# Optimization experiments

Hardware: AMD Instinct MI355X
Metric: run time of the kernel (lower is better)

The kernel has to match this reference:

```python
import jax, jax.numpy as jnp
import numpy as np

B, C, H, W = 16, 256, 64, 32
HID = C // 8  # down_ratio = 8
NEG = -9e15   # masking constant from the original code


def _spatial_adj(h, w):
    # 8-connected grid adjacency over n = h*w pixels (no self loops), as bool [n, n]
    ii, jj = np.meshgrid(np.arange(h), np.arange(w), indexing='ij')
    pi, pj = ii.reshape(-1), jj.reshape(-1)
    di = np.abs(pi[:, None] - pi[None, :])
    dj = np.abs(pj[:, None] - pj[None, :])
    return (di <= 1) & (dj <= 1) & ~((di == 0) & (dj == 0))


def _channel_adj(c):
    # chain adjacency over channels: |i - j| == 1, bool [c, c]
    i = np.arange(c)
    return np.abs(i[:, None] - i[None, :]) == 1


def setup_inputs() -> dict:
    key = jax.random.key(0)
    ks = jax.random.split(key, 12)
    return {
        'x': jax.random.normal(ks[0], (B, C, H, W), dtype=jnp.float32),
        'wa': jax.random.normal(ks[1], (HID, C), dtype=jnp.float32) * 0.05,
        'ga': jax.random.uniform(ks[2], (HID,), dtype=jnp.float32) + 0.5,
        'ba': jax.random.normal(ks[3], (HID,), dtype=jnp.float32) * 0.1,
        'ma': jnp.zeros((HID,), dtype=jnp.float32),
        'va': jnp.ones((HID,), dtype=jnp.float32),
        'ws': jax.random.normal(ks[4], (HID, C), dtype=jnp.float32) * 0.05,
        'gs': jax.random.uniform(ks[5], (HID,), dtype=jnp.float32) + 0.5,
        'bs': jax.random.normal(ks[6], (HID,), dtype=jnp.float32) * 0.1,
        'ms': jnp.zeros((HID,), dtype=jnp.float32),
        'vs': jnp.ones((HID,), dtype=jnp.float32),
        'gama': jax.random.uniform(ks[7], (1,), dtype=jnp.float32),
    }


def _bn_relu(y, g, b, m, v):
    # eval-mode BatchNorm2d (+ReLU) on [B, k, H, W]
    inv = g / jnp.sqrt(v + 1e-5)
    return jax.nn.relu(y * inv[:, None, None] + (b - m * inv)[:, None, None])


def reference(x, wa, ga, ba, ma, va, ws, gs, bs, ms, vs, gama):
    b, c, h, w = x.shape
    n = h * w
    adj = jnp.asarray(_spatial_adj(h, w))   # [n, n] bool (constant)
    cadj = jnp.asarray(_channel_adj(c))     # [c, c] bool (constant)

    # spatial GAT branch
    alpha = _bn_relu(jnp.einsum('bchw,oc->bohw', x, wa), ga, ba, ma, va)
    sigma = _bn_relu(jnp.einsum('bchw,oc->bohw', x, ws), gs, bs, ms, vs)
    xf = x.reshape(b, c, n)
    af = alpha.reshape(b, -1, n)            # [b, hid, n]
    sf = sigma.reshape(b, -1, n)            # [b, hid, n]
    att = jnp.einsum('bkn,bkm->bnm', af, sf)              # [b, n, n]
    att = jax.nn.softmax(jnp.where(adj, att, NEG), axis=2)
    h_s = jnp.einsum('bnm,bcm->bcn', att, xf).reshape(b, c, h, w)

    # channel GAT branch
    Gc = jnp.einsum('bcn,bdn->bcd', xf, xf)               # [b, c, c]
    catt = jax.nn.softmax(jnp.where(cadj, Gc, NEG), axis=2)
    h_p = jnp.einsum('bcd,bdn->bcn', catt, xf).reshape(b, c, h, w)

    h_prime = jax.nn.elu(h_s + h_p)
    return (1.0 - gama) * x + gama * h_prime
```

## Files before the change

### kernel.cpp

```cpp
#include <hip/hip_runtime.h>
#include <math.h>

#define BB 16
#define CC 256
#define HH 64
#define WW 32
#define NN (HH*WW)
#define NEGC (-9e15f)
#define CPAD 136

typedef __attribute__((ext_vector_type(8))) short bf16x8;
typedef __attribute__((ext_vector_type(4))) float f32x4;

__device__ float g_wlo[BB*CC];
__device__ float g_whi[BB*CC];
__device__ float g_as[(size_t)BB*NN*64];
__device__ float g_part[BB*32*256];
__device__ float g_w8[(size_t)BB*NN*8];

__device__ __forceinline__ unsigned short f2bf(float f) {
    unsigned int u = __float_as_uint(f);
    u += 0x7FFFu + ((u >> 16) & 1u);
    return (unsigned short)(u >> 16);
}

__global__ __launch_bounds__(256) void k_gemm(
        const float* __restrict__ x,
        const float* __restrict__ wa, const float* __restrict__ ga,
        const float* __restrict__ va, const float* __restrict__ ba,
        const float* __restrict__ ma, const float* __restrict__ wsig,
        const float* __restrict__ gs, const float* __restrict__ vs,
        const float* __restrict__ bs, const float* __restrict__ ms) {
    __shared__ unsigned short xbuf[64*CPAD];
    __shared__ unsigned short wbuf[64*CPAD];
    int blk = blockIdx.x;
    int b = blk >> 5, tile = blk & 31;
    int t = threadIdx.x;
    int p0 = tile*64;
    const float* xb = x + (size_t)b*CC*NN + p0;

    int kw = t >> 2, sub = t & 3;
    const float* wrow; float g_, v_;
    if (kw < 32) { g_ = ga[kw]; v_ = va[kw]; wrow = wa + kw*CC; }
    else         { g_ = gs[kw-32]; v_ = vs[kw-32]; wrow = wsig + (kw-32)*CC; }
    float invk = g_ * rsqrtf(v_ + 1e-5f);

    int g = t >> 4, q = t & 15;
    int wv_ = t >> 6;
    int lane = t & 63;
    int pcol = lane & 15, grp = lane >> 4;

    f32x4 acc[4];
    #pragma unroll
    for (int i = 0; i < 4; ++i) acc[i] = (f32x4){0.f, 0.f, 0.f, 0.f};

    #pragma unroll
    for (int h = 0; h < 2; ++h) {
        if (h) __syncthreads();
        float pp[8];
        #pragma unroll
        for (int i = 0; i < 8; ++i) pp[i] = 0.f;
        float4 prev = make_float4(0.f, 0.f, 0.f, 0.f);
        #pragma unroll
        for (int i = 0; i <= 8; ++i) {
            int c = h*128 + g*8 + i;
            float4 v = make_float4(0.f, 0.f, 0.f, 0.f);
            if (c < CC) v = *(const float4*)(xb + (size_t)c*NN + q*4);
            if (i < 8) {
                int cl = g*8 + i;
                xbuf[(q*4+0)*CPAD + cl] = f2bf(v.x);
                xbuf[(q*4+1)*CPAD + cl] = f2bf(v.y);
                xbuf[(q*4+2)*CPAD + cl] = f2bf(v.z);
                xbuf[(q*4+3)*CPAD + cl] = f2bf(v.w);
            }
            if (i > 0) {
                pp[i-1] = fmaf(prev.x, v.x, pp[i-1]);
                pp[i-1] = fmaf(prev.y, v.y, pp[i-1]);
                pp[i-1] = fmaf(prev.z, v.z, pp[i-1]);
                pp[i-1] = fmaf(prev.w, v.w, pp[i-1]);
            }
            prev = v;
        }
        float myv = 0.f;
        #pragma unroll
        for (int i = 0; i < 8; ++i) {
            float r = pp[i];
            r += __shfl_xor(r, 1, 64);
            r += __shfl_xor(r, 2, 64);
            r += __shfl_xor(r, 4, 64);
            r += __shfl_xor(r, 8, 64);
            if (q == i) myv = r;
        }
        if (q < 8) {
            int c = h*128 + g*8 + q;
            g_part[(b*32 + tile)*256 + c] = myv;
        }
        #pragma unroll
        for (int m = 0; m < 8; ++m) {
            int cl = sub*32 + m*4;
            float4 w4 = *(const float4*)(wrow + h*128 + cl);
            unsigned int pk0 = (unsigned int)f2bf(w4.x*invk) |
                               ((unsigned int)f2bf(w4.y*invk) << 16);
            unsigned int pk1 = (unsigned int)f2bf(w4.z*invk) |
                               ((unsigned int)f2bf(w4.w*invk) << 16);
            *(unsigned int*)&wbuf[kw*CPAD + cl]     = pk0;
            *(unsigned int*)&wbuf[kw*CPAD + cl + 2] = pk1;
        }
        __syncthreads();
        #pragma unroll
        for (int cs = 0; cs < 4; ++cs) {
            int c_off = cs*32 + grp*8;
            bf16x8 bfrag = *(const bf16x8*)&xbuf[(wv_*16 + pcol)*CPAD + c_off];
            #pragma unroll
            for (int kt = 0; kt < 4; ++kt) {
                bf16x8 afrag = *(const bf16x8*)&wbuf[(kt*16 + pcol)*CPAD + c_off];
                acc[kt] = __builtin_amdgcn_mfma_f32_16x16x32_bf16(afrag, bfrag, acc[kt], 0, 0, 0);
            }
        }
    }

    #pragma unroll
    for (int kt = 0; kt < 4; ++kt) {
        int k0 = kt*16 + grp*4;
        float4 gv, vv, bv, mv;
        if (k0 < 32) {
            gv = *(const float4*)(ga + k0); vv = *(const float4*)(va + k0);
            bv = *(const float4*)(ba + k0); mv = *(const float4*)(ma + k0);
        } else {
            gv = *(const float4*)(gs + k0-32); vv = *(const float4*)(vs + k0-32);
            bv = *(const float4*)(bs + k0-32); mv = *(const float4*)(ms + k0-32);
        }
        float i0 = gv.x * rsqrtf(vv.x + 1e-5f);
        float i1 = gv.y * rsqrtf(vv.y + 1e-5f);
        float i2 = gv.z * rsqrtf(vv.z + 1e-5f);
        float i3 = gv.w * rsqrtf(vv.w + 1e-5f);
        float4 r;
        r.x = fmaxf(acc[kt][0] + (bv.x - mv.x*i0), 0.f);
        r.y = fmaxf(acc[kt][1] + (bv.y - mv.y*i1), 0.f);
        r.z = fmaxf(acc[kt][2] + (bv.z - mv.z*i2), 0.f);
        r.w = fmaxf(acc[kt][3] + (bv.w - mv.w*i3), 0.f);
        *(float4*)(g_as + (((size_t)(b*NN + p0 + wv_*16 + pcol)) << 6) + k0) = r;
    }
}

#define WBLK (BB*NN/32)
__global__ __launch_bounds__(256) void k_wc() {
    __shared__ float lds_s[256];
    int blk = blockIdx.x;
    int t = threadIdx.x;
    if (blk < WBLK) {
        int pos_local = t >> 3, j = t & 7;
        int idx = blk*32 + pos_local;
        int b = idx >> 11, p = idx & (NN-1);
        int gr = p >> 5, col = p & 31;
        const int dy[8] = {-1,-1,-1, 0,0, 1,1,1};
        const int dx[8] = {-1, 0, 1,-1,1,-1,0,1};
        int qr = gr + dy[j], qc = col + dx[j];
        bool ok = (qr >= 0) && (qr < HH) && (qc >= 0) && (qc < WW);
        int q = ok ? (qr*WW + qc) : p;
        const float4* ap = (const float4*)(g_as + (((size_t)b*NN + p) << 6));
        const float4* sp = (const float4*)(g_as + (((size_t)b*NN + q) << 6) + 32);
        float d = 0.f;
        #pragma unroll
        for (int k4 = 0; k4 < 8; ++k4) {
            float4 a = ap[k4], s = sp[k4];
            d = fmaf(a.x, s.x, d); d = fmaf(a.y, s.y, d);
            d = fmaf(a.z, s.z, d); d = fmaf(a.w, s.w, d);
        }
        float logit = ok ? d : NEGC;
        float m = logit;
        m = fmaxf(m, __shfl_xor(m, 1, 64));
        m = fmaxf(m, __shfl_xor(m, 2, 64));
        m = fmaxf(m, __shfl_xor(m, 4, 64));
        float e = expf(logit - m);
        float s8 = e;
        s8 += __shfl_xor(s8, 1, 64);
        s8 += __shfl_xor(s8, 2, 64);
        s8 += __shfl_xor(s8, 4, 64);
        g_w8[(size_t)idx*8 + j] = e / s8;
    } else {
        int b = blk - WBLK;
        float s = 0.f;
        #pragma unroll 8
        for (int tile = 0; tile < 32; ++tile) s += g_part[(b*32 + tile)*256 + t];
        lds_s[t] = s;
        __syncthreads();
        int c = t;
        float glo = (c > 0)      ? lds_s[c-1] : NEGC;
        float ghi = (c < CC - 1) ? lds_s[c]   : NEGC;
        float m = fmaxf(glo, ghi);
        float elo = expf(glo - m), ehi = expf(ghi - m);
        float inv = 1.0f / (elo + ehi);
        g_wlo[b*CC + c] = elo * inv;
        g_whi[b*CC + c] = ehi * inv;
    }
}

__global__ __launch_bounds__(256) void k_main(const float* __restrict__ x,
                                              const float* __restrict__ gama_p,
                                              float* __restrict__ out) {
    __shared__ float xt[18*10*36];
    int blk = blockIdx.x;
    int b = blk >> 7;
    int strip = (blk >> 4) & 7;
    int cg = blk & 15;
    int t = threadIdx.x;
    int r0 = strip << 3;
    int c0 = cg << 4;
    const float* xb = x + (size_t)b*CC*NN;

    int wave = __builtin_amdgcn_readfirstlane(t >> 6);
    int lane = t & 63;
    int lrow = lane >> 3;
    int lcq  = (lane & 7) << 2;

    float wq[4][8];
    {
        const float4* wp = (const float4*)(g_w8 +
            ((size_t)(b*NN + r0*WW + lrow*WW + lcq)) * 8);
        #pragma unroll
        for (int i = 0; i < 4; ++i) {
            float4 w0 = wp[2*i], w1 = wp[2*i+1];
            wq[i][0]=w0.x; wq[i][1]=w0.y; wq[i][2]=w0.z; wq[i][3]=w0.w;
            wq[i][4]=w1.x; wq[i][5]=w1.y; wq[i][6]=w1.z; wq[i][7]=w1.w;
        }
    }

    for (int i = t; i < 1440; i += 256) {
        int seg = i >> 3, quad = i & 7;
        int ch_s = seg / 10, r_s = seg - ch_s*10;
        int gc = c0 - 1 + ch_s;  gc = (gc < 0) ? 0 : (gc > CC-1 ? CC-1 : gc);
        int gr = r0 - 1 + r_s;   gr = (gr < 0) ? 0 : (gr > HH-1 ? HH-1 : gr);
        float4 v = *(const float4*)(xb + (size_t)gc*NN + gr*WW + quad*4);
        *(float4*)(&xt[(ch_s*10 + r_s)*36 + quad*4]) = v;
    }
    __syncthreads();

    float gama = gama_p[0];
    int cw0 = wave*4;
    int pbase = r0*WW + lane*4;
    float* ob = out + (size_t)b*CC*NN;

    float pm1[4], o0[4];
    {
        float4 v = *(const float4*)(&xt[((cw0+0)*10 + (lrow+1))*36 + lcq]);
        pm1[0]=v.x; pm1[1]=v.y; pm1[2]=v.z; pm1[3]=v.w;
        float4 w = *(const float4*)(&xt[((cw0+1)*10 + (lrow+1))*36 + lcq]);
        o0[0]=w.x; o0[1]=w.y; o0[2]=w.z; o0[3]=w.w;
    }
    #pragma unroll
    for (int cc = 0; cc < 4; ++cc) {
        int c = c0 + cw0 + cc;
        int slot = cw0 + 1 + cc;
        float4 v1 = *(const float4*)(&xt[((slot+1)*10 + (lrow+1))*36 + lcq]);
        float p1[4] = {v1.x, v1.y, v1.z, v1.w};
        float4 va4 = *(const float4*)(&xt[(slot*10 + lrow    )*36 + lcq]);
        float aw[4] = {va4.x, va4.y, va4.z, va4.w};
        float4 vb4 = *(const float4*)(&xt[(slot*10 + lrow + 2)*36 + lcq]);
        float bw[4] = {vb4.x, vb4.y, vb4.z, vb4.w};
        float al  = __shfl_up(aw[3], 1);
        float ar  = __shfl_down(aw[0], 1);
        float ol  = __shfl_up(o0[3], 1);
        float orr = __shfl_down(o0[0], 1);
        float bl  = __shfl_up(bw[3], 1);
        float br  = __shfl_down(bw[0], 1);
        float wlo_c = g_wlo[b*CC + c];
        float whi_c = g_whi[b*CC + c];
        float res[4];
        #pragma unroll
        for (int i = 0; i < 4; ++i) {
            float ul = (i == 0) ? al  : aw[i-1];
            float uu = aw[i];
            float ur = (i == 3) ? ar  : aw[i+1];
            float ll = (i == 0) ? ol  : o0[i-1];
            float rr = (i == 3) ? orr : o0[i+1];
            float dl = (i == 0) ? bl  : bw[i-1];
            float dd = bw[i];
            float dr = (i == 3) ? br  : bw[i+1];
            float hs = wq[i][0]*ul + wq[i][1]*uu + wq[i][2]*ur
                     + wq[i][3]*ll + wq[i][4]*rr
                     + wq[i][5]*dl + wq[i][6]*dd + wq[i][7]*dr;
            float hp = wlo_c*pm1[i] + whi_c*p1[i];
            float h  = hs + hp;
            float el = (h > 0.f) ? h : expm1f(h);
            res[i] = o0[i] + gama*(el - o0[i]);
        }
        *(float4*)(ob + (size_t)c*NN + pbase) = make_float4(res[0], res[1], res[2], res[3]);
        #pragma unroll
        for (int i = 0; i < 4; ++i) { pm1[i] = o0[i]; o0[i] = p1[i]; }
    }
}

extern "C" void kernel_launch(void* const* d_in, const int* in_sizes, int n_in,
                              void* d_out, int out_size, void* d_ws, size_t ws_size,
                              hipStream_t stream) {
    const float* x    = (const float*)d_in[0];
    const float* wa   = (const float*)d_in[1];
    const float* ga   = (const float*)d_in[2];
    const float* ba   = (const float*)d_in[3];
    const float* ma   = (const float*)d_in[4];
    const float* va   = (const float*)d_in[5];
    const float* wsig = (const float*)d_in[6];
    const float* gs   = (const float*)d_in[7];
    const float* bs   = (const float*)d_in[8];
    const float* ms   = (const float*)d_in[9];
    const float* vs   = (const float*)d_in[10];
    const float* gama = (const float*)d_in[11];
    float* out = (float*)d_out;

    hipLaunchKernelGGL(k_gemm, dim3(512),      dim3(256), 0, stream,
                       x, wa, ga, va, ba, ma, wsig, gs, vs, bs, ms);
    hipLaunchKernelGGL(k_wc,   dim3(WBLK+BB),  dim3(256), 0, stream);
    hipLaunchKernelGGL(k_main, dim3(2048),     dim3(256), 0, stream, x, gama, out);
}
```

Measured before the change: 49.92 us.

## Fuse attention-weight kernel into main stencil kernel with row-strip channel loop

Removes the separate k_wc kernel. Each k_main block now computes its own 8-neighbour spatial softmax weights for a 2-row strip and the per-channel chain softmax, keeping both in LDS instead of round-tripping through global g_w8/g_wlo/g_whi. Blocks are remapped to cover 2 rows × all 256 channels, looping over 16 channel chunks with a small halo tile reloaded per chunk. This saves a launch and global traffic. In exchange the grid shrinks to 512 blocks, the vertical halo overhead is larger, the channel softmax is recomputed redundantly per block, and two barriers are added per chunk.

```diff
diff --git a/kernel.cpp b/kernel.cpp
--- a/kernel.cpp
+++ b/kernel.cpp
@@ -12,11 +12,8 @@
 typedef __attribute__((ext_vector_type(8))) short bf16x8;
 typedef __attribute__((ext_vector_type(4))) float f32x4;
 
-__device__ float g_wlo[BB*CC];
-__device__ float g_whi[BB*CC];
 __device__ float g_as[(size_t)BB*NN*64];
 __device__ float g_part[BB*32*256];
-__device__ float g_w8[(size_t)BB*NN*8];
 
 __device__ __forceinline__ unsigned short f2bf(float f) {
     unsigned int u = __float_as_uint(f);
@@ -143,120 +140,109 @@
     }
 }
 
-#define WBLK (BB*NN/32)
-__global__ __launch_bounds__(256) void k_wc() {
-    __shared__ float lds_s[256];
-    int blk = blockIdx.x;
-    int t = threadIdx.x;
-    if (blk < WBLK) {
-        int pos_local = t >> 3, j = t & 7;
-        int idx = blk*32 + pos_local;
-        int b = idx >> 11, p = idx & (NN-1);
-        int gr = p >> 5, col = p & 31;
-        const int dy[8] = {-1,-1,-1, 0,0, 1,1,1};
-        const int dx[8] = {-1, 0, 1,-1,1,-1,0,1};
-        int qr = gr + dy[j], qc = col + dx[j];
-        bool ok = (qr >= 0) && (qr < HH) && (qc >= 0) && (qc < WW);
-        int q = ok ? (qr*WW + qc) : p;
-        const float4* ap = (const float4*)(g_as + (((size_t)b*NN + p) << 6));
-        const float4* sp = (const float4*)(g_as + (((size_t)b*NN + q) << 6) + 32);
-        float d = 0.f;
-        #pragma unroll
-        for (int k4 = 0; k4 < 8; ++k4) {
-            float4 a = ap[k4], s = sp[k4];
-            d = fmaf(a.x, s.x, d); d = fmaf(a.y, s.y, d);
-            d = fmaf(a.z, s.z, d); d = fmaf(a.w, s.w, d);
-        }
-        float logit = ok ? d : NEGC;
-        float m = logit;
-        m = fmaxf(m, __shfl_xor(m, 1, 64));
-        m = fmaxf(m, __shfl_xor(m, 2, 64));
-        m = fmaxf(m, __shfl_xor(m, 4, 64));
-        float e = expf(logit - m);
-        float s8 = e;
-        s8 += __shfl_xor(s8, 1, 64);
-        s8 += __shfl_xor(s8, 2, 64);
-        s8 += __shfl_xor(s8, 4, 64);
-        g_w8[(size_t)idx*8 + j] = e / s8;
-    } else {
-        int b = blk - WBLK;
-        float s = 0.f;
-        #pragma unroll 8
-        for (int tile = 0; tile < 32; ++tile) s += g_part[(b*32 + tile)*256 + t];
-        lds_s[t] = s;
-        __syncthreads();
-        int c = t;
-        float glo = (c > 0)      ? lds_s[c-1] : NEGC;
-        float ghi = (c < CC - 1) ? lds_s[c]   : NEGC;
-        float m = fmaxf(glo, ghi);
-        float elo = expf(glo - m), ehi = expf(ghi - m);
-        float inv = 1.0f / (elo + ehi);
-        g_wlo[b*CC + c] = elo * inv;
-        g_whi[b*CC + c] = ehi * inv;
-    }
-}
-
 __global__ __launch_bounds__(256) void k_main(const float* __restrict__ x,
                                               const float* __restrict__ gama_p,
                                               float* __restrict__ out) {
-    __shared__ float xt[18*10*36];
+    __shared__ float wlo_s[256];
+    __shared__ float whi_s[256];
+    __shared__ float wtab[64*9];
+    __shared__ float xt[18*4*36];
     int blk = blockIdx.x;
-    int b = blk >> 7;
-    int strip = (blk >> 4) & 7;
-    int cg = blk & 15;
+    int b = blk >> 5, st = blk & 31;
+    int r0 = st*2;
     int t = threadIdx.x;
-    int r0 = strip << 3;
-    int c0 = cg << 4;
+
+    {
+        float s = 0.f;
+        #pragma unroll 8
+        for (int tl = 0; tl < 32; ++tl) s += g_part[(b*32 + tl)*256 + t];
+        xt[t] = s;
+    }
+    {
+        const int dy[8] = {-1,-1,-1, 0,0, 1,1,1};
+        const int dx[8] = {-1, 0, 1,-1,1,-1,0,1};
+        int j = t & 7;
+        #pragma unroll
+        for (int it = 0; it < 2; ++it) {
+            int pl = it*32 + (t >> 3);
+            int prow = pl >> 5, pcol = pl & 31;
+            int gr = r0 + prow;
+            int p = gr*WW + pcol;
+            int qr = gr + dy[j], qc = pcol + dx[j];
+            bool ok = (qr >= 0) && (qr < HH) && (qc >= 0) && (qc < WW);
+            int q = ok ? (qr*WW + qc) : p;
+            const float4* ap = (const float4*)(g_as + (((size_t)b*NN + p) << 6));
+            const float4* sp = (const float4*)(g_as + (((size_t)b*NN + q) << 6) + 32);
+            float d = 0.f;
+            #pragma unroll
+            for (int k4 = 0; k4 < 8; ++k4) {
+                float4 a = ap[k4], s4 = sp[k4];
+                d = fmaf(a.x, s4.x, d); d = fmaf(a.y, s4.y, d);
+                d = fmaf(a.z, s4.z, d); d = fmaf(a.w, s4.w, d);
+            }
+            float logit = ok ? d : NEGC;
+            float m = logit;
+            m = fmaxf(m, __shfl_xor(m, 1, 64));
+            m = fmaxf(m, __shfl_xor(m, 2, 64));
+            m = fmaxf(m, __shfl_xor(m, 4, 64));
+            float e = expf(logit - m);
+            float s8 = e;
+            s8 += __shfl_xor(s8, 1, 64);
+            s8 += __shfl_xor(s8, 2, 64);
+            s8 += __shfl_xor(s8, 4, 64);
+            wtab[pl*9 + j] = e / s8;
+        }
+    }
+    __syncthreads();
+    {
+        float glo = (t > 0)      ? xt[t-1] : NEGC;
+        float ghi = (t < CC - 1) ? xt[t]   : NEGC;
+        float m = fmaxf(glo, ghi);
+        float elo = expf(glo - m), ehi = expf(ghi - m);
+        float iv = 1.0f / (elo + ehi);
+        wlo_s[t] = elo * iv;
+        whi_s[t] = ehi * iv;
+    }
+    int ch_l = t >> 4;
+    int s16  = t & 15;
+    int lrow = s16 >> 3;
+    int quad = s16 & 7;
+    int lcq  = quad*4;
+    float wq[4][8];
+    #pragma unroll
+    for (int i = 0; i < 4; ++i) {
+        int pl = lrow*32 + lcq + i;
+        #pragma unroll
+        for (int j = 0; j < 8; ++j) wq[i][j] = wtab[pl*9 + j];
+    }
+    float gama = gama_p[0];
     const float* xb = x + (size_t)b*CC*NN;
-
-    int wave = __builtin_amdgcn_readfirstlane(t >> 6);
-    int lane = t & 63;
-    int lrow = lane >> 3;
-    int lcq  = (lane & 7) << 2;
-
-    float wq[4][8];
-    {
-        const float4* wp = (const float4*)(g_w8 +
-            ((size_t)(b*NN + r0*WW + lrow*WW + lcq)) * 8);
-        #pragma unroll
-        for (int i = 0; i < 4; ++i) {
-            float4 w0 = wp[2*i], w1 = wp[2*i+1];
-            wq[i][0]=w0.x; wq[i][1]=w0.y; wq[i][2]=w0.z; wq[i][3]=w0.w;
-            wq[i][4]=w1.x; wq[i][5]=w1.y; wq[i][6]=w1.z; wq[i][7]=w1.w;
-        }
-    }
-
-    for (int i = t; i < 1440; i += 256) {
-        int seg = i >> 3, quad = i & 7;
-        int ch_s = seg / 10, r_s = seg - ch_s*10;
-        int gc = c0 - 1 + ch_s;  gc = (gc < 0) ? 0 : (gc > CC-1 ? CC-1 : gc);
-        int gr = r0 - 1 + r_s;   gr = (gr < 0) ? 0 : (gr > HH-1 ? HH-1 : gr);
-        float4 v = *(const float4*)(xb + (size_t)gc*NN + gr*WW + quad*4);
-        *(float4*)(&xt[(ch_s*10 + r_s)*36 + quad*4]) = v;
-    }
-    __syncthreads();
-
-    float gama = gama_p[0];
-    int cw0 = wave*4;
-    int pbase = r0*WW + lane*4;
     float* ob = out + (size_t)b*CC*NN;
 
-    float pm1[4], o0[4];
-    {
-        float4 v = *(const float4*)(&xt[((cw0+0)*10 + (lrow+1))*36 + lcq]);
-        pm1[0]=v.x; pm1[1]=v.y; pm1[2]=v.z; pm1[3]=v.w;
-        float4 w = *(const float4*)(&xt[((cw0+1)*10 + (lrow+1))*36 + lcq]);
-        o0[0]=w.x; o0[1]=w.y; o0[2]=w.z; o0[3]=w.w;
-    }
-    #pragma unroll
-    for (int cc = 0; cc < 4; ++cc) {
-        int c = c0 + cw0 + cc;
-        int slot = cw0 + 1 + cc;
-        float4 v1 = *(const float4*)(&xt[((slot+1)*10 + (lrow+1))*36 + lcq]);
+    for (int chunk = 0; chunk < 16; ++chunk) {
+        __syncthreads();
+        int c0 = chunk*16;
+        for (int i = t; i < 576; i += 256) {
+            int seg = i >> 3, q8 = i & 7;
+            int ch_s = seg >> 2, r_s = seg & 3;
+            int gc = c0 - 1 + ch_s;  gc = (gc < 0) ? 0 : (gc > CC-1 ? CC-1 : gc);
+            int gr = r0 - 1 + r_s;   gr = (gr < 0) ? 0 : (gr > HH-1 ? HH-1 : gr);
+            *(float4*)&xt[seg*36 + q8*4] =
+                *(const float4*)(xb + (size_t)gc*NN + gr*WW + q8*4);
+        }
+        __syncthreads();
+
+        int slot = ch_l + 1;
+        int c = c0 + ch_l;
+        float4 vm = *(const float4*)&xt[((slot-1)*4 + lrow+1)*36 + lcq];
+        float pm1[4] = {vm.x, vm.y, vm.z, vm.w};
+        float4 vo = *(const float4*)&xt[( slot   *4 + lrow+1)*36 + lcq];
+        float o0[4] = {vo.x, vo.y, vo.z, vo.w};
+        float4 v1 = *(const float4*)&xt[((slot+1)*4 + lrow+1)*36 + lcq];
         float p1[4] = {v1.x, v1.y, v1.z, v1.w};
-        float4 va4 = *(const float4*)(&xt[(slot*10 + lrow    )*36 + lcq]);
+        float4 va4 = *(const float4*)&xt[( slot   *4 + lrow  )*36 + lcq];
         float aw[4] = {va4.x, va4.y, va4.z, va4.w};
-        float4 vb4 = *(const float4*)(&xt[(slot*10 + lrow + 2)*36 + lcq]);
+        float4 vb4 = *(const float4*)&xt[( slot   *4 + lrow+2)*36 + lcq];
         float bw[4] = {vb4.x, vb4.y, vb4.z, vb4.w};
         float al  = __shfl_up(aw[3], 1);
         float ar  = __shfl_down(aw[0], 1);
@@ -264,8 +250,8 @@
         float orr = __shfl_down(o0[0], 1);
         float bl  = __shfl_up(bw[3], 1);
         float br  = __shfl_down(bw[0], 1);
-        float wlo_c = g_wlo[b*CC + c];
-        float whi_c = g_whi[b*CC + c];
+        float wlo_c = wlo_s[c];
+        float whi_c = whi_s[c];
         float res[4];
         #pragma unroll
         for (int i = 0; i < 4; ++i) {
@@ -285,9 +271,8 @@
             float el = (h > 0.f) ? h : expm1f(h);
             res[i] = o0[i] + gama*(el - o0[i]);
         }
-        *(float4*)(ob + (size_t)c*NN + pbase) = make_float4(res[0], res[1], res[2], res[3]);
-        #pragma unroll
-        for (int i = 0; i < 4; ++i) { pm1[i] = o0[i]; o0[i] = p1[i]; }
+        *(float4*)(ob + (size_t)c*NN + (r0+lrow)*WW + lcq) =
+            make_float4(res[0], res[1], res[2], res[3]);
     }
 }
 
@@ -308,8 +293,7 @@
     const float* gama = (const float*)d_in[11];
     float* out = (float*)d_out;
 
-    hipLaunchKernelGGL(k_gemm, dim3(512),      dim3(256), 0, stream,
+    hipLaunchKernelGGL(k_gemm, dim3(512), dim3(256), 0, stream,
                        x, wa, ga, va, ba, ma, wsig, gs, vs, bs, ms);
-    hipLaunchKernelGGL(k_wc,   dim3(WBLK+BB),  dim3(256), 0, stream);
-    hipLaunchKernelGGL(k_main, dim3(2048),     dim3(256), 0, stream, x, gama, out);
-}
+    hipLaunchKernelGGL(k_main, dim3(512), dim3(256), 0, stream, x, gama, out);
+}
```

New measurement: 57.21 us. 1.15x slower.
